# Optimization experiments

Hardware: AMD Instinct MI355X
Metric: run time of the kernel (lower is better)

The kernel has to match this reference:

```python
import jax, jax.numpy as jnp
import numpy as np

N, E = 50000, 800000
IN_DIM, OUT_DIM, H = 256, 128, 8
GEO_HID = 16  # RBF feature dim and geo_mlp hidden dim


def setup_inputs() -> dict:
    key = jax.random.key(0)
    ks = jax.random.split(key, 16)
    def lin(k, fan_out, fan_in):
        kw, kb = jax.random.split(k)
        lim = 1.0 / np.sqrt(fan_in)
        W = jax.random.uniform(kw, (fan_out, fan_in), jnp.float32, -lim, lim)
        b = jax.random.uniform(kb, (fan_out,), jnp.float32, -lim, lim)
        return W, b
    Wq, bq = lin(ks[0], OUT_DIM, IN_DIM)
    Wk, bk = lin(ks[1], OUT_DIM, IN_DIM)
    Wv, bv = lin(ks[2], OUT_DIM, IN_DIM)
    Wo, bo = lin(ks[3], OUT_DIM, OUT_DIM)
    Wg1, bg1 = lin(ks[4], GEO_HID, GEO_HID)
    Wg2, bg2 = lin(ks[5], H, GEO_HID)
    x = jax.random.normal(ks[6], (N, IN_DIM), jnp.float32)
    edge_index = jax.random.randint(ks[7], (2, E), 0, N, jnp.int64)
    edge_dist = jax.random.uniform(ks[8], (E,), jnp.float32) * 6.0
    return {"x": x, "edge_index": edge_index, "edge_dist": edge_dist,
            "Wq": Wq, "bq": bq, "Wk": Wk, "bk": bk, "Wv": Wv, "bv": bv,
            "Wo": Wo, "bo": bo, "Wg1": Wg1, "bg1": bg1, "Wg2": Wg2, "bg2": bg2}


def reference(x, edge_index, edge_dist, Wq, bq, Wk, bk, Wv, bv, Wo, bo, Wg1, bg1, Wg2, bg2):
    n = x.shape[0]
    num_heads = Wg2.shape[0]
    head_dim = Wq.shape[0] // num_heads
    scale = 1.0 / (head_dim ** 0.5)

    q = (x @ Wq.T + bq).reshape(n, num_heads, head_dim)
    k = (x @ Wk.T + bk).reshape(n, num_heads, head_dim)
    v = (x @ Wv.T + bv).reshape(n, num_heads, head_dim)

    # RBF expansion: 16 centers in [0, 6], gamma = 1.0
    centers = jnp.linspace(0.0, 6.0, GEO_HID)
    rbf = jnp.exp(-(edge_dist[:, None] - centers) ** 2)          # [E, 16]
    geo_bias = jax.nn.relu(rbf @ Wg1.T + bg1) @ Wg2.T + bg2      # [E, H]

    row, col = edge_index[0], edge_index[1]
    attn = (q[row] * k[col]).sum(-1) * scale + geo_bias          # [E, H]

    # segment softmax over incoming edges per destination node (row)
    m = jax.ops.segment_max(attn, row, num_segments=n)           # [N, H]
    e = jnp.exp(attn - m[row])
    s = jax.ops.segment_sum(e, row, num_segments=n)              # [N, H]
    a = e / (s[row] + 1e-12)                                     # [E, H]

    out = jax.ops.segment_sum(v[col] * a[:, :, None], row, num_segments=n)
    out = out.reshape(n, num_heads * head_dim)
    return out @ Wo.T + bo
```

## Files before the change

kernel.cpp:

```cpp
#include <hip/hip_runtime.h>
#include <math.h>

#define IN_DIM 256
#define OUT_DIM 128
#define NH 8
#define HD 16
#define GH 16
#define TBL 1024
#define LOG2E 1.44269504f
#define RCAP 64
#define BCAP 2560

typedef __attribute__((ext_vector_type(8))) short short8;
typedef __attribute__((ext_vector_type(4))) float floatx4;

__device__ __forceinline__ unsigned short f2bf(float f) {
    union { float f; unsigned u; } v; v.f = f;
    unsigned r = v.u + 0x7fffu + ((v.u >> 16) & 1u);
    return (unsigned short)(r >> 16);
}
__device__ __forceinline__ float bf2f(unsigned short h) {
    union { unsigned u; float f; } v; v.u = ((unsigned)h) << 16;
    return v.f;
}
__device__ __forceinline__ void split1(float f, unsigned short& h, unsigned short& l) {
    h = f2bf(f);
    l = f2bf(f - bf2f(h));
}
__device__ __forceinline__ float bflo(unsigned u) { return __uint_as_float(u << 16); }
__device__ __forceinline__ float bfhi(unsigned u) { return __uint_as_float(u & 0xffff0000u); }

__global__ __launch_bounds__(256) void prep_all_kernel(
    const float* __restrict__ x, const float* __restrict__ Wq, const float* __restrict__ Wk,
    const float* __restrict__ Wv, const float* __restrict__ Wo,
    unsigned short* __restrict__ xh, unsigned short* __restrict__ xl,
    unsigned short* __restrict__ wh, unsigned short* __restrict__ wl,
    unsigned short* __restrict__ wo_h, unsigned short* __restrict__ wo_l,
    const float* __restrict__ Wg1, const float* __restrict__ bg1,
    const float* __restrict__ Wg2, const float* __restrict__ bg2,
    float* __restrict__ tbl, int* __restrict__ gbin,
    int n4x, int nbins, int nsplit, int nwm, int nwo, int ngeo) {
    int bx = blockIdx.x;
    int t = threadIdx.x;

    if (bx < nsplit) {
        int i = bx * 256 + t;
        if (i >= n4x) return;
        float4 f = ((const float4*)x)[i];
        ushort4 h, l;
        split1(f.x, h.x, l.x); split1(f.y, h.y, l.y);
        split1(f.z, h.z, l.z); split1(f.w, h.w, l.w);
        ((ushort4*)xh)[i] = h;
        ((ushort4*)xl)[i] = l;
        return;
    }
    bx -= nsplit;
    if (bx < 3 * nwm) {
        int m = bx / nwm;
        int i = (bx - m * nwm) * 256 + t;
        if (i >= (OUT_DIM * IN_DIM) / 4) return;
        const float* W = (m == 0) ? Wq : (m == 1) ? Wk : Wv;
        float4 f = ((const float4*)W)[i];
        ushort4 h, l;
        split1(f.x, h.x, l.x); split1(f.y, h.y, l.y);
        split1(f.z, h.z, l.z); split1(f.w, h.w, l.w);
        size_t base = (size_t)m * (OUT_DIM * IN_DIM) / 4;
        ((ushort4*)wh)[base + i] = h;
        ((ushort4*)wl)[base + i] = l;
        return;
    }
    bx -= 3 * nwm;
    if (bx < nwo) {
        int i = bx * 256 + t;
        if (i >= (OUT_DIM * OUT_DIM) / 4) return;
        float4 f = ((const float4*)Wo)[i];
        ushort4 h, l;
        split1(f.x, h.x, l.x); split1(f.y, h.y, l.y);
        split1(f.z, h.z, l.z); split1(f.w, h.w, l.w);
        ((ushort4*)wo_h)[i] = h;
        ((ushort4*)wo_l)[i] = l;
        return;
    }
    bx -= nwo;
    if (bx < ngeo) {
        int i = bx * 256 + t;
        if (i >= TBL) return;
        float d = (float)i * (6.0f / (float)(TBL - 1));
        float rbf[GH];
#pragma unroll
        for (int j = 0; j < GH; ++j) {
            float c = 0.4f * (float)j;
            float tt = d - c;
            rbf[j] = __expf(-tt * tt);
        }
        float hid[GH];
#pragma unroll
        for (int j = 0; j < GH; ++j) {
            float acc = bg1[j];
#pragma unroll
            for (int kk = 0; kk < GH; ++kk) acc += rbf[kk] * Wg1[j * GH + kk];
            hid[j] = fmaxf(acc, 0.0f);
        }
#pragma unroll
        for (int h = 0; h < NH; ++h) {
            float acc = bg2[h];
#pragma unroll
            for (int j = 0; j < GH; ++j) acc += hid[j] * Wg2[h * GH + j];
            tbl[i * NH + h] = acc * LOG2E;
        }
        return;
    }
    for (int i = t; i < nbins; i += 256) gbin[i] = 0;
}

__global__ __launch_bounds__(512, 4) void qkv_kernel(
    const unsigned short* __restrict__ xh, const unsigned short* __restrict__ xl,
    const unsigned short* __restrict__ wh, const unsigned short* __restrict__ wl,
    const float* __restrict__ bq, const float* __restrict__ bk, const float* __restrict__ bv,
    float* __restrict__ q, unsigned short* __restrict__ kb, unsigned short* __restrict__ vb,
    const int* __restrict__ ei, const float* __restrict__ edist,
    int* __restrict__ gbin, int2* __restrict__ binbuf,
    int Nn, int E_, int nxb, int nb1, int nbins) {
    __shared__ unsigned short xh_s[128 * 40];
    __shared__ unsigned short xl_s[128 * 40];
    __shared__ unsigned short wh_s[128 * 40];
    __shared__ unsigned short wl_s[128 * 40];

    const int tid = threadIdx.x;
    int bx = blockIdx.x;

    if (bx < nb1) {
        int* hist = (int*)xh_s;
        const int e0 = bx * 4096;
        for (int b = tid; b < nbins; b += 512) hist[b] = 0;
        __syncthreads();
#pragma unroll
        for (int i = 0; i < 8; ++i) {
            int e = e0 + tid + i * 512;
            if (e < E_) atomicAdd(&hist[ei[e] >> 7], 1);
        }
        __syncthreads();
        for (int b = tid; b < nbins; b += 512) {
            int h = hist[b];
            int base = 0;
            if (h) base = atomicAdd(&gbin[b], h);
            hist[b] = base;
        }
        __syncthreads();
#pragma unroll
        for (int i = 0; i < 8; ++i) {
            int e = e0 + tid + i * 512;
            if (e < E_) {
                int row = ei[e];
                int bin = row >> 7;
                int r = atomicAdd(&hist[bin], 1);
                float u = edist[e] * ((float)(TBL - 1) / 6.0f);
                u = fminf(fmaxf(u, 0.0f), (float)(TBL - 1));
                if (r < BCAP)
                    binbuf[(size_t)bin * BCAP + r] =
                        make_int2((ei[E_ + e] & 0x1FFFF) | ((row & 127) << 17), __float_as_int(u));
            }
        }
        return;
    }
    bx -= nb1;

    const int wsel = bx / nxb;
    const int n0 = (bx - wsel * nxb) * 128;
    const unsigned short* W_h = wh + (size_t)wsel * (OUT_DIM * IN_DIM);
    const unsigned short* W_l = wl + (size_t)wsel * (OUT_DIM * IN_DIM);
    const float* bias = (wsel == 0) ? bq : (wsel == 1) ? bk : bv;
    const bool vpath = (wsel == 2);

    const int w = tid >> 6;
    const int lane = tid & 63;
    const int ml = lane & 15;
    const int quad = lane >> 4;
    const int rg = w & 3;
    const int cg = w >> 2;

    const int rows_valid = min(128, Nn - n0);

    floatx4 acc[2][4];
#pragma unroll
    for (int rr = 0; rr < 2; ++rr)
#pragma unroll
        for (int ct = 0; ct < 4; ++ct) acc[rr][ct] = (floatx4){0.f, 0.f, 0.f, 0.f};

    const short8 zero8 = {0, 0, 0, 0, 0, 0, 0, 0};

    for (int kc = 0; kc < IN_DIM; kc += 32) {
        {
            int r = tid >> 2, c = tid & 3;
            size_t gx = (size_t)(n0 + r) * IN_DIM + kc + c * 8;
            size_t gw = (size_t)r * IN_DIM + kc + c * 8;
            short8 vh = zero8;
            if (r < rows_valid) vh = *(const short8*)(xh + gx);
            *(short8*)(xh_s + r * 40 + c * 8) = vh;
            *(short8*)(wh_s + r * 40 + c * 8) = *(const short8*)(W_h + gw);
            if (vpath) {
                short8 vl = zero8;
                if (r < rows_valid) vl = *(const short8*)(xl + gx);
                *(short8*)(xl_s + r * 40 + c * 8) = vl;
                *(short8*)(wl_s + r * 40 + c * 8) = *(const short8*)(W_l + gw);
            }
        }
        __syncthreads();

        short8 ah0 = *(const short8*)(xh_s + (rg * 32 + ml) * 40 + quad * 8);
        short8 ah1 = *(const short8*)(xh_s + (rg * 32 + 16 + ml) * 40 + quad * 8);
        if (!vpath) {
#pragma unroll
            for (int ct = 0; ct < 4; ++ct) {
                short8 bh = *(const short8*)(wh_s + (cg * 64 + ct * 16 + ml) * 40 + quad * 8);
                acc[0][ct] = __builtin_amdgcn_mfma_f32_16x16x32_bf16(ah0, bh, acc[0][ct], 0, 0, 0);
                acc[1][ct] = __builtin_amdgcn_mfma_f32_16x16x32_bf16(ah1, bh, acc[1][ct], 0, 0, 0);
            }
        } else {
            short8 al0 = *(const short8*)(xl_s + (rg * 32 + ml) * 40 + quad * 8);
            short8 al1 = *(const short8*)(xl_s + (rg * 32 + 16 + ml) * 40 + quad * 8);
#pragma unroll
            for (int ct = 0; ct < 4; ++ct) {
                short8 bh = *(const short8*)(wh_s + (cg * 64 + ct * 16 + ml) * 40 + quad * 8);
                short8 bl = *(const short8*)(wl_s + (cg * 64 + ct * 16 + ml) * 40 + quad * 8);
                acc[0][ct] = __builtin_amdgcn_mfma_f32_16x16x32_bf16(ah0, bh, acc[0][ct], 0, 0, 0);
                acc[0][ct] = __builtin_amdgcn_mfma_f32_16x16x32_bf16(al0, bh, acc[0][ct], 0, 0, 0);
                acc[0][ct] = __builtin_amdgcn_mfma_f32_16x16x32_bf16(ah0, bl, acc[0][ct], 0, 0, 0);
                acc[1][ct] = __builtin_amdgcn_mfma_f32_16x16x32_bf16(ah1, bh, acc[1][ct], 0, 0, 0);
                acc[1][ct] = __builtin_amdgcn_mfma_f32_16x16x32_bf16(al1, bh, acc[1][ct], 0, 0, 0);
                acc[1][ct] = __builtin_amdgcn_mfma_f32_16x16x32_bf16(ah1, bl, acc[1][ct], 0, 0, 0);
            }
        }
        __syncthreads();
    }

    if (wsel == 0) {
#pragma unroll
        for (int rr = 0; rr < 2; ++rr)
#pragma unroll
            for (int ct = 0; ct < 4; ++ct) {
                int col = cg * 64 + ct * 16 + ml;
                float bj = bias[col];
#pragma unroll
                for (int r = 0; r < 4; ++r) {
                    int grow = n0 + rg * 32 + rr * 16 + quad * 4 + r;
                    if (grow < Nn) q[(size_t)grow * 128 + col] = acc[rr][ct][r] + bj;
                }
            }
    } else {
        unsigned short* ob = (wsel == 1) ? kb : vb;
#pragma unroll
        for (int rr = 0; rr < 2; ++rr)
#pragma unroll
            for (int ct = 0; ct < 4; ++ct) {
                int col = cg * 64 + ct * 16 + ml;
                float bj = bias[col];
#pragma unroll
                for (int r = 0; r < 4; ++r) {
                    int grow = n0 + rg * 32 + rr * 16 + quad * 4 + r;
                    if (grow < Nn) ob[(size_t)grow * 128 + col] = f2bf(acc[rr][ct][r] + bj);
                }
            }
    }
}

__global__ __launch_bounds__(256) void bin2bucket_kernel(
    const int2* __restrict__ binbuf, const int* __restrict__ gbin,
    int2* __restrict__ bucket, int* __restrict__ rowstart, int* __restrict__ cnt, int Nn) {
    __shared__ int rcnt[128];
    __shared__ int pref[128];
    __shared__ int2 ebuf[BCAP];
    const int bin = blockIdx.x;
    const int t = threadIdx.x;
    if (t < 128) rcnt[t] = 0;
    __syncthreads();
    int nb = gbin[bin];
    if (nb > BCAP) nb = BCAP;
    const int row0 = bin << 7;

    int px[10], py[10], rk[10];
#pragma unroll
    for (int j = 0; j < 10; ++j) {
        int i = t + j * 256;
        rk[j] = -1;
        if (i < nb) {
            int2 p = binbuf[(size_t)bin * BCAP + i];
            int rowrel = (p.x >> 17) & 127;
            int r = atomicAdd(&rcnt[rowrel], 1);
            if (r < RCAP) { px[j] = p.x & 0x1FFFF; py[j] = p.y; rk[j] = r | (rowrel << 16); }
        }
    }
    __syncthreads();
    int myclamp = 0;
    if (t < 128) { myclamp = min(rcnt[t], RCAP); pref[t] = myclamp; }
    __syncthreads();
    for (int off = 1; off < 128; off <<= 1) {
        int v = 0;
        if (t < 128 && t >= off) v = pref[t - off];
        __syncthreads();
        if (t < 128) pref[t] += v;
        __syncthreads();
    }
#pragma unroll
    for (int j = 0; j < 10; ++j) {
        if (rk[j] >= 0) {
            int rowrel = rk[j] >> 16;
            int r = rk[j] & 0xFFFF;
            int pos = pref[rowrel] - min(rcnt[rowrel], RCAP) + r;
            ebuf[pos] = make_int2(px[j], py[j]);
        }
    }
    __syncthreads();
    int total = pref[127];
    const int obase = bin * BCAP;
    for (int i = t; i < total; i += 256) bucket[obase + i] = ebuf[i];
    if (t < 128 && row0 + t < Nn) {
        rowstart[row0 + t] = obase + pref[t] - myclamp;
        cnt[row0 + t] = myclamp;
    }
}

__global__ __launch_bounds__(256) void fused_node_kernel(
    const float* __restrict__ q, const unsigned short* __restrict__ kb,
    const unsigned short* __restrict__ vb, const int2* __restrict__ bucket,
    const float* __restrict__ tbl, const int* __restrict__ rowstart, const int* __restrict__ cnt,
    float* __restrict__ o, int Nn) {
    int lane = threadIdx.x & 63;
    int n = blockIdx.x * 4 + (threadIdx.x >> 6);
    if (n >= Nn) return;
    int g = lane >> 3;
    int h = lane & 7;
    int start = rowstart[n];
    int end = start + cnt[n];

    float qf[16];
    {
        const float4* qp = (const float4*)(q + (size_t)n * 128 + h * 16);
#pragma unroll
        for (int j = 0; j < 4; ++j) {
            float4 t = qp[j];
            qf[j * 4 + 0] = t.x; qf[j * 4 + 1] = t.y;
            qf[j * 4 + 2] = t.z; qf[j * 4 + 3] = t.w;
        }
    }

    float l = 0.0f;
    float acc[16];
#pragma unroll
    for (int j = 0; j < 16; ++j) acc[j] = 0.0f;

    int2 np;
    if (start < end) np = bucket[min(start + g, end - 1)];

#pragma unroll 2
    for (int base = start; base < end; base += 8) {
        bool valid = (base + g < end);
        int2 cur = np;
        int nxt = base + 8;
        if (nxt < end) np = bucket[min(nxt + g, end - 1)];

        int col = cur.x;
        float u = __int_as_float(cur.y);

        const uint4* kp = (const uint4*)(kb + (size_t)col * 128 + h * 16);
        uint4 k0 = kp[0], k1 = kp[1];
        const uint4* vp = (const uint4*)(vb + (size_t)col * 128 + h * 16);
        uint4 v0 = vp[0], v1 = vp[1];

        unsigned kk[8] = {k0.x, k0.y, k0.z, k0.w, k1.x, k1.y, k1.z, k1.w};
        float d = 0.0f;
#pragma unroll
        for (int j = 0; j < 8; ++j) {
            d = fmaf(bflo(kk[j]), qf[2 * j], d);
            d = fmaf(bfhi(kk[j]), qf[2 * j + 1], d);
        }

        int i0 = min((int)u, TBL - 2);
        float fr = u - (float)i0;
        float t0 = tbl[i0 * NH + h];
        float t1 = tbl[i0 * NH + NH + h];
        float logit2 = fmaf(d, 0.25f * LOG2E, fmaf(fr, t1 - t0, t0));
        logit2 = fminf(logit2, 80.0f);
        if (!valid) logit2 = -1e30f;
        float p = __builtin_amdgcn_exp2f(logit2);

        l += p;
        unsigned vv[8] = {v0.x, v0.y, v0.z, v0.w, v1.x, v1.y, v1.z, v1.w};
#pragma unroll
        for (int j = 0; j < 8; ++j) {
            acc[2 * j]     = fmaf(p, bflo(vv[j]), acc[2 * j]);
            acc[2 * j + 1] = fmaf(p, bfhi(vv[j]), acc[2 * j + 1]);
        }
    }

#pragma unroll
    for (int off = 8; off < 64; off <<= 1) {
        l += __shfl_xor(l, off);
#pragma unroll
        for (int j = 0; j < 16; ++j) acc[j] += __shfl_xor(acc[j], off);
    }

    if (g == 0) {
        float inv = 1.0f / (l + 1e-12f);
        float4* op = (float4*)(o + (size_t)n * 128 + h * 16);
#pragma unroll
        for (int j = 0; j < 4; ++j) {
            float4 t;
            t.x = acc[j * 4 + 0] * inv; t.y = acc[j * 4 + 1] * inv;
            t.z = acc[j * 4 + 2] * inv; t.w = acc[j * 4 + 3] * inv;
            op[j] = t;
        }
    }
}

__global__ __launch_bounds__(512, 4) void out_gemm_mfma_kernel(
    const float* __restrict__ o,
    const unsigned short* __restrict__ wo_h, const unsigned short* __restrict__ wo_l,
    const float* __restrict__ bo, float* __restrict__ out, int Nn) {
    const int n0 = blockIdx.x * 128;

    __shared__ unsigned short xh_s[128 * 40];
    __shared__ unsigned short xl_s[128 * 40];
    __shared__ unsigned short wh_s[128 * 40];
    __shared__ unsigned short wl_s[128 * 40];

    const int tid = threadIdx.x;
    const int w = tid >> 6;
    const int lane = tid & 63;
    const int ml = lane & 15;
    const int quad = lane >> 4;
    const int rg = w & 3;
    const int cg = w >> 2;

    const int rows_valid = min(128, Nn - n0);

    floatx4 acc[2][4];
#pragma unroll
    for (int rr = 0; rr < 2; ++rr)
#pragma unroll
        for (int ct = 0; ct < 4; ++ct) acc[rr][ct] = (floatx4){0.f, 0.f, 0.f, 0.f};

    for (int kc = 0; kc < OUT_DIM; kc += 32) {
        {
            int r = tid >> 2, c = tid & 3;
            unsigned short hv[8], lv[8];
            if (r < rows_valid) {
                const float* src = o + (size_t)(n0 + r) * OUT_DIM + kc + c * 8;
#pragma unroll
                for (int j = 0; j < 8; ++j) split1(src[j], hv[j], lv[j]);
            } else {
#pragma unroll
                for (int j = 0; j < 8; ++j) { hv[j] = 0; lv[j] = 0; }
            }
            *(short8*)(xh_s + r * 40 + c * 8) = *(short8*)hv;
            *(short8*)(xl_s + r * 40 + c * 8) = *(short8*)lv;
            size_t gg = (size_t)r * OUT_DIM + kc + c * 8;
            *(short8*)(wh_s + r * 40 + c * 8) = *(const short8*)(wo_h + gg);
            *(short8*)(wl_s + r * 40 + c * 8) = *(const short8*)(wo_l + gg);
        }
        __syncthreads();

        short8 ah0 = *(const short8*)(xh_s + (rg * 32 + ml) * 40 + quad * 8);
        short8 ah1 = *(const short8*)(xh_s + (rg * 32 + 16 + ml) * 40 + quad * 8);
        short8 al0 = *(const short8*)(xl_s + (rg * 32 + ml) * 40 + quad * 8);
        short8 al1 = *(const short8*)(xl_s + (rg * 32 + 16 + ml) * 40 + quad * 8);
#pragma unroll
        for (int ct = 0; ct < 4; ++ct) {
            short8 bh = *(const short8*)(wh_s + (cg * 64 + ct * 16 + ml) * 40 + quad * 8);
            short8 bl = *(const short8*)(wl_s + (cg * 64 + ct * 16 + ml) * 40 + quad * 8);
            acc[0][ct] = __builtin_amdgcn_mfma_f32_16x16x32_bf16(ah0, bh, acc[0][ct], 0, 0, 0);
            acc[0][ct] = __builtin_amdgcn_mfma_f32_16x16x32_bf16(al0, bh, acc[0][ct], 0, 0, 0);
            acc[0][ct] = __builtin_amdgcn_mfma_f32_16x16x32_bf16(ah0, bl, acc[0][ct], 0, 0, 0);
            acc[1][ct] = __builtin_amdgcn_mfma_f32_16x16x32_bf16(ah1, bh, acc[1][ct], 0, 0, 0);
            acc[1][ct] = __builtin_amdgcn_mfma_f32_16x16x32_bf16(al1, bh, acc[1][ct], 0, 0, 0);
            acc[1][ct] = __builtin_amdgcn_mfma_f32_16x16x32_bf16(ah1, bl, acc[1][ct], 0, 0, 0);
        }
        __syncthreads();
    }

#pragma unroll
    for (int rr = 0; rr < 2; ++rr)
#pragma unroll
        for (int ct = 0; ct < 4; ++ct) {
            int col = cg * 64 + ct * 16 + ml;
            float bj = bo[col];
#pragma unroll
            for (int r = 0; r < 4; ++r) {
                int grow = n0 + rg * 32 + rr * 16 + quad * 4 + r;
                if (grow < Nn) out[(size_t)grow * 128 + col] = acc[rr][ct][r] + bj;
            }
        }
}

extern "C" void kernel_launch(void* const* d_in, const int* in_sizes, int n_in,
                              void* d_out, int out_size, void* d_ws, size_t ws_size,
                              hipStream_t stream) {
    const float* x   = (const float*)d_in[0];
    const int* ei    = (const int*)d_in[1];
    const float* edist = (const float*)d_in[2];
    const float* Wq = (const float*)d_in[3];  const float* bq = (const float*)d_in[4];
    const float* Wk = (const float*)d_in[5];  const float* bk = (const float*)d_in[6];
    const float* Wv = (const float*)d_in[7];  const float* bv = (const float*)d_in[8];
    const float* Wo = (const float*)d_in[9];  const float* bo = (const float*)d_in[10];
    const float* Wg1 = (const float*)d_in[11]; const float* bg1 = (const float*)d_in[12];
    const float* Wg2 = (const float*)d_in[13]; const float* bg2 = (const float*)d_in[14];
    const int Nn = in_sizes[0] / IN_DIM;
    const int Ee = in_sizes[2];
    float* out = (float*)d_out;

    char* ws = (char*)d_ws;
    size_t off = 0;
    auto alloc = [&](size_t bytes) -> char* {
        char* p = ws + off;
        off += (bytes + 255) & ~(size_t)255;
        return p;
    };
    float* q  = (float*)alloc((size_t)Nn * 128 * 4);
    unsigned short* kbuf = (unsigned short*)alloc((size_t)Nn * 128 * 2);
    unsigned short* vbuf = (unsigned short*)alloc((size_t)Nn * 128 * 2);
    char* xlblock = alloc((size_t)Nn * IN_DIM * 2);
    float* o = (float*)alloc((size_t)Nn * 128 * 4);
    float* geot = (float*)alloc((size_t)TBL * 8 * 4);
    int* cnt = (int*)alloc((size_t)Nn * 4);
    int* rowstart = (int*)alloc((size_t)Nn * 4);
    int nbins = (Nn + 127) >> 7;
    int* gbin = (int*)alloc((size_t)nbins * 4);
    unsigned short* wh_all = (unsigned short*)alloc((size_t)3 * OUT_DIM * IN_DIM * 2);
    unsigned short* wl_all = (unsigned short*)alloc((size_t)3 * OUT_DIM * IN_DIM * 2);
    unsigned short* wo_h = (unsigned short*)alloc((size_t)OUT_DIM * OUT_DIM * 2);
    unsigned short* wo_l = (unsigned short*)alloc((size_t)OUT_DIM * OUT_DIM * 2);
    int2* bucket = (int2*)alloc((size_t)nbins * BCAP * 8);

    int2* binbuf = (int2*)o;

    unsigned short* xh = (unsigned short*)d_out;
    unsigned short* xl = (unsigned short*)xlblock;

    int n4x = Nn * IN_DIM / 4;
    int nsplit = (n4x + 255) / 256;
    int nwm = ((OUT_DIM * IN_DIM / 4) + 255) / 256;
    int nwo = ((OUT_DIM * OUT_DIM / 4) + 255) / 256;
    int ngeo = (TBL + 255) / 256;
    int gprep = nsplit + 3 * nwm + nwo + ngeo + 1;
    prep_all_kernel<<<gprep, 256, 0, stream>>>(
        x, Wq, Wk, Wv, Wo, xh, xl, wh_all, wl_all, wo_h, wo_l,
        Wg1, bg1, Wg2, bg2, geot, gbin, n4x, nbins, nsplit, nwm, nwo, ngeo);

    int nxb = (Nn + 127) / 128;
    int nb1 = (Ee + 4095) / 4096;
    qkv_kernel<<<nb1 + 3 * nxb, 512, 0, stream>>>(
        xh, xl, wh_all, wl_all, bq, bk, bv, q, kbuf, vbuf,
        ei, edist, gbin, binbuf, Nn, Ee, nxb, nb1, nbins);

    bin2bucket_kernel<<<nbins, 256, 0, stream>>>(binbuf, gbin, bucket, rowstart, cnt, Nn);

    fused_node_kernel<<<(Nn + 3) / 4, 256, 0, stream>>>(q, kbuf, vbuf, bucket, geot, rowstart, cnt, o, Nn);

    out_gemm_mfma_kernel<<<(Nn + 127) / 128, 512, 0, stream>>>(o, wo_h, wo_l, bo, out, Nn);
}
```

Measured before the change: 270.7 us.

## Make node attention kernel persistent with packed row metadata and two-batch prefetch

```diff
diff --git a/kernel.cpp b/kernel.cpp
--- a/kernel.cpp
+++ b/kernel.cpp
@@ -266,7 +266,7 @@
 
 __global__ __launch_bounds__(256) void bin2bucket_kernel(
     const int2* __restrict__ binbuf, const int* __restrict__ gbin,
-    int2* __restrict__ bucket, int* __restrict__ rowstart, int* __restrict__ cnt, int Nn) {
+    int2* __restrict__ bucket, int2* __restrict__ meta, int Nn) {
     __shared__ int rcnt[128];
     __shared__ int pref[128];
     __shared__ int2 ebuf[BCAP];
@@ -314,101 +314,121 @@
     int total = pref[127];
     const int obase = bin * BCAP;
     for (int i = t; i < total; i += 256) bucket[obase + i] = ebuf[i];
-    if (t < 128 && row0 + t < Nn) {
-        rowstart[row0 + t] = obase + pref[t] - myclamp;
-        cnt[row0 + t] = myclamp;
-    }
+    if (t < 128 && row0 + t < Nn)
+        meta[row0 + t] = make_int2(obase + pref[t] - myclamp, myclamp);
 }
 
 __global__ __launch_bounds__(256) void fused_node_kernel(
     const float* __restrict__ q, const unsigned short* __restrict__ kb,
     const unsigned short* __restrict__ vb, const int2* __restrict__ bucket,
-    const float* __restrict__ tbl, const int* __restrict__ rowstart, const int* __restrict__ cnt,
-    float* __restrict__ o, int Nn) {
-    int lane = threadIdx.x & 63;
-    int n = blockIdx.x * 4 + (threadIdx.x >> 6);
-    if (n >= Nn) return;
-    int g = lane >> 3;
-    int h = lane & 7;
-    int start = rowstart[n];
-    int end = start + cnt[n];
-
-    float qf[16];
-    {
-        const float4* qp = (const float4*)(q + (size_t)n * 128 + h * 16);
-#pragma unroll
-        for (int j = 0; j < 4; ++j) {
-            float4 t = qp[j];
-            qf[j * 4 + 0] = t.x; qf[j * 4 + 1] = t.y;
-            qf[j * 4 + 2] = t.z; qf[j * 4 + 3] = t.w;
-        }
-    }
-
-    float l = 0.0f;
-    float acc[16];
-#pragma unroll
-    for (int j = 0; j < 16; ++j) acc[j] = 0.0f;
-
-    int2 np;
-    if (start < end) np = bucket[min(start + g, end - 1)];
-
-#pragma unroll 2
-    for (int base = start; base < end; base += 8) {
-        bool valid = (base + g < end);
-        int2 cur = np;
-        int nxt = base + 8;
-        if (nxt < end) np = bucket[min(nxt + g, end - 1)];
-
-        int col = cur.x;
-        float u = __int_as_float(cur.y);
-
-        const uint4* kp = (const uint4*)(kb + (size_t)col * 128 + h * 16);
-        uint4 k0 = kp[0], k1 = kp[1];
-        const uint4* vp = (const uint4*)(vb + (size_t)col * 128 + h * 16);
-        uint4 v0 = vp[0], v1 = vp[1];
-
-        unsigned kk[8] = {k0.x, k0.y, k0.z, k0.w, k1.x, k1.y, k1.z, k1.w};
-        float d = 0.0f;
-#pragma unroll
-        for (int j = 0; j < 8; ++j) {
-            d = fmaf(bflo(kk[j]), qf[2 * j], d);
-            d = fmaf(bfhi(kk[j]), qf[2 * j + 1], d);
-        }
-
-        int i0 = min((int)u, TBL - 2);
-        float fr = u - (float)i0;
-        float t0 = tbl[i0 * NH + h];
-        float t1 = tbl[i0 * NH + NH + h];
-        float logit2 = fmaf(d, 0.25f * LOG2E, fmaf(fr, t1 - t0, t0));
-        logit2 = fminf(logit2, 80.0f);
-        if (!valid) logit2 = -1e30f;
-        float p = __builtin_amdgcn_exp2f(logit2);
-
-        l += p;
-        unsigned vv[8] = {v0.x, v0.y, v0.z, v0.w, v1.x, v1.y, v1.z, v1.w};
-#pragma unroll
-        for (int j = 0; j < 8; ++j) {
-            acc[2 * j]     = fmaf(p, bflo(vv[j]), acc[2 * j]);
-            acc[2 * j + 1] = fmaf(p, bfhi(vv[j]), acc[2 * j + 1]);
-        }
-    }
-
-#pragma unroll
-    for (int off = 8; off < 64; off <<= 1) {
-        l += __shfl_xor(l, off);
-#pragma unroll
-        for (int j = 0; j < 16; ++j) acc[j] += __shfl_xor(acc[j], off);
-    }
-
-    if (g == 0) {
-        float inv = 1.0f / (l + 1e-12f);
-        float4* op = (float4*)(o + (size_t)n * 128 + h * 16);
-#pragma unroll
-        for (int j = 0; j < 4; ++j) {
-            float4 t;
-            t.x = acc[j * 4 + 0] * inv; t.y = acc[j * 4 + 1] * inv;
-            t.z = acc[j * 4 + 2] * inv; t.w = acc[j * 4 + 3] * inv;
-            op[j] = t;
+    const float* __restrict__ tbl, const int2* __restrict__ meta,
+    float* __restrict__ o, int Nn, int nwav) {
+    const int lane = threadIdx.x & 63;
+    const int g = lane >> 3;
+    const int h = lane & 7;
+    int wid = blockIdx.x * (blockDim.x >> 6) + (threadIdx.x >> 6);
+    if (wid >= Nn) return;
+
+    int2 mnext = meta[wid];
+    for (int n = wid; n < Nn; n += nwav) {
+        const int2 m = mnext;
+        const int n2 = n + nwav;
+        if (n2 < Nn) mnext = meta[n2];
+
+        const int start = m.x;
+        const int c = m.y;
+        const int end = start + c;
+
+        float qf[16];
+        {
+            const float4* qp = (const float4*)(q + (size_t)n * 128 + h * 16);
+#pragma unroll
+            for (int j = 0; j < 4; ++j) {
+                float4 t = qp[j];
+                qf[j * 4 + 0] = t.x; qf[j * 4 + 1] = t.y;
+                qf[j * 4 + 2] = t.z; qf[j * 4 + 3] = t.w;
+            }
+        }
+
+        float l = 0.0f;
+        float acc[16];
+#pragma unroll
+        for (int j = 0; j < 16; ++j) acc[j] = 0.0f;
+
+        auto edge_math = [&](const uint4& k0, const uint4& k1, const uint4& v0, const uint4& v1,
+                             float u, bool valid) {
+            unsigned kk[8] = {k0.x, k0.y, k0.z, k0.w, k1.x, k1.y, k1.z, k1.w};
+            float d = 0.0f;
+#pragma unroll
+            for (int j = 0; j < 8; ++j) {
+                d = fmaf(bflo(kk[j]), qf[2 * j], d);
+                d = fmaf(bfhi(kk[j]), qf[2 * j + 1], d);
+            }
+            int i0 = min((int)u, TBL - 2);
+            float fr = u - (float)i0;
+            float t0 = tbl[i0 * NH + h];
+            float t1 = tbl[i0 * NH + NH + h];
+            float logit2 = fmaf(d, 0.25f * LOG2E, fmaf(fr, t1 - t0, t0));
+            logit2 = fminf(logit2, 80.0f);
+            if (!valid) logit2 = -1e30f;
+            float p = __builtin_amdgcn_exp2f(logit2);
+            l += p;
+            unsigned vv[8] = {v0.x, v0.y, v0.z, v0.w, v1.x, v1.y, v1.z, v1.w};
+#pragma unroll
+            for (int j = 0; j < 8; ++j) {
+                acc[2 * j]     = fmaf(p, bflo(vv[j]), acc[2 * j]);
+                acc[2 * j + 1] = fmaf(p, bfhi(vv[j]), acc[2 * j + 1]);
+            }
+        };
+
+        if (c > 0) {
+            int2 npA = bucket[min(start + g, end - 1)];
+            const bool vAv = (start + g < end);
+            const bool doB = (end > start + 8);
+            int2 npB = npA;
+            bool vBv = false;
+            if (doB) {
+                npB = bucket[min(start + 8 + g, end - 1)];
+                vBv = (start + 8 + g < end);
+            }
+            const uint4* kpA = (const uint4*)(kb + (size_t)npA.x * 128 + h * 16);
+            const uint4* vpA = (const uint4*)(vb + (size_t)npA.x * 128 + h * 16);
+            uint4 kA0 = kpA[0], kA1 = kpA[1], vA0 = vpA[0], vA1 = vpA[1];
+            uint4 kB0, kB1, vB0, vB1;
+            if (doB) {
+                const uint4* kpB = (const uint4*)(kb + (size_t)npB.x * 128 + h * 16);
+                const uint4* vpB = (const uint4*)(vb + (size_t)npB.x * 128 + h * 16);
+                kB0 = kpB[0]; kB1 = kpB[1]; vB0 = vpB[0]; vB1 = vpB[1];
+            }
+            edge_math(kA0, kA1, vA0, vA1, __int_as_float(npA.y), vAv);
+            if (doB) edge_math(kB0, kB1, vB0, vB1, __int_as_float(npB.y), vBv);
+            for (int base = start + 16; base < end; base += 8) {
+                int2 np = bucket[min(base + g, end - 1)];
+                bool valid = (base + g < end);
+                const uint4* kp = (const uint4*)(kb + (size_t)np.x * 128 + h * 16);
+                const uint4* vp = (const uint4*)(vb + (size_t)np.x * 128 + h * 16);
+                uint4 k0 = kp[0], k1 = kp[1], v0 = vp[0], v1 = vp[1];
+                edge_math(k0, k1, v0, v1, __int_as_float(np.y), valid);
+            }
+        }
+
+#pragma unroll
+        for (int off = 8; off < 64; off <<= 1) {
+            l += __shfl_xor(l, off);
+#pragma unroll
+            for (int j = 0; j < 16; ++j) acc[j] += __shfl_xor(acc[j], off);
+        }
+
+        if (g == 0) {
+            float inv = 1.0f / (l + 1e-12f);
+            float4* op = (float4*)(o + (size_t)n * 128 + h * 16);
+#pragma unroll
+            for (int j = 0; j < 4; ++j) {
+                float4 t;
+                t.x = acc[j * 4 + 0] * inv; t.y = acc[j * 4 + 1] * inv;
+                t.z = acc[j * 4 + 2] * inv; t.w = acc[j * 4 + 3] * inv;
+                op[j] = t;
+            }
         }
     }
 }
@@ -521,8 +541,7 @@
     char* xlblock = alloc((size_t)Nn * IN_DIM * 2);
     float* o = (float*)alloc((size_t)Nn * 128 * 4);
     float* geot = (float*)alloc((size_t)TBL * 8 * 4);
-    int* cnt = (int*)alloc((size_t)Nn * 4);
-    int* rowstart = (int*)alloc((size_t)Nn * 4);
+    int2* meta = (int2*)alloc((size_t)Nn * 8);
     int nbins = (Nn + 127) >> 7;
     int* gbin = (int*)alloc((size_t)nbins * 4);
     unsigned short* wh_all = (unsigned short*)alloc((size_t)3 * OUT_DIM * IN_DIM * 2);
@@ -552,9 +571,13 @@
         xh, xl, wh_all, wl_all, bq, bk, bv, q, kbuf, vbuf,
         ei, edist, gbin, binbuf, Nn, Ee, nxb, nb1, nbins);
 
-    bin2bucket_kernel<<<nbins, 256, 0, stream>>>(binbuf, gbin, bucket, rowstart, cnt, Nn);
-
-    fused_node_kernel<<<(Nn + 3) / 4, 256, 0, stream>>>(q, kbuf, vbuf, bucket, geot, rowstart, cnt, o, Nn);
+    bin2bucket_kernel<<<nbins, 256, 0, stream>>>(binbuf, gbin, bucket, meta, Nn);
+
+    {
+        int nblk = 2048;
+        int nwav = nblk * 4;
+        fused_node_kernel<<<nblk, 256, 0, stream>>>(q, kbuf, vbuf, bucket, geot, meta, o, Nn, nwav);
+    }
 
     out_gemm_mfma_kernel<<<(Nn + 127) / 128, 512, 0, stream>>>(o, wo_h, wo_l, bo, out, Nn);
 }
```

New measurement: 267.7 us. No clear change (-1.1%).
